# Performance work log

Measured on AMD Instinct MI355X. Metric: run time of the kernel, lower is better.

Reference implementation:

```python
import jax, jax.numpy as jnp
import numpy as np

DEPTH = 6
N_LEAVES = 2 ** DEPTH


def setup_inputs() -> dict:
    key = jax.random.key(0)
    ks = jax.random.split(key, 7)
    in_f, lw, out_f = 1024, 64, 512
    B = 4096
    s1 = 1.0 / np.sqrt(in_f)
    s2 = 1.0 / np.sqrt(lw)
    return {
        "x": jax.random.normal(ks[0], (B, in_f), jnp.float32),
        "node_weights": jax.random.uniform(ks[1], (N_LEAVES - 1, in_f), jnp.float32, -s1, s1),
        "node_biases": jax.random.uniform(ks[2], (N_LEAVES - 1, 1), jnp.float32, -s1, s1),
        "w1s": jax.random.uniform(ks[3], (N_LEAVES, in_f, lw), jnp.float32, -s1, s1),
        "b1s": jax.random.uniform(ks[4], (N_LEAVES, lw), jnp.float32, -s1, s1),
        "w2s": jax.random.uniform(ks[5], (N_LEAVES, lw, out_f), jnp.float32, -s2, s2),
        "b2s": jax.random.uniform(ks[6], (N_LEAVES, out_f), jnp.float32, -s2, s2),
    }


def _fff_forward(x, node_weights, node_biases, w1s, b1s, w2s, b2s):
    B = x.shape[0]
    # Soft routing: build per-leaf mixture weights level by level (training path).
    mixture = jnp.ones((B, N_LEAVES), x.dtype)
    for d in range(DEPTH):
        platform = 2 ** d - 1
        n_nodes = 2 ** d
        w = node_weights[platform:platform + n_nodes]          # (n, in)
        b = node_biases[platform:platform + n_nodes]            # (n, 1)
        logits = x @ w.T + b.T                                  # (B, n)
        be = jax.nn.sigmoid(logits)
        mod = jnp.stack([1.0 - be, be], axis=-1).reshape(B, 2 * n_nodes)
        mixture = (mixture.reshape(B, 2 * n_nodes, N_LEAVES // (2 * n_nodes))
                   * mod[:, :, None]).reshape(B, N_LEAVES)
    # All-leaf expert MLPs (grouped GEMMs), then mixture-weighted sum.
    h = jax.nn.relu(jnp.einsum('bi,liw->blw', x, w1s) + b1s[None])   # (B, L, W)
    y = jnp.einsum('blw,lwo->blo', h, w2s) + b2s[None]                # (B, L, O)
    return jnp.sum(y * mixture[:, :, None], axis=1)                   # (B, O)


def reference(x, node_weights, node_biases, w1s, b1s, w2s, b2s):
    return _fff_forward(x, node_weights, node_biases, w1s, b1s, w2s, b2s)
```

## Files before the change

kernel.cpp:

```cpp
#include <hip/hip_runtime.h>
#include <hip/hip_bf16.h>

typedef unsigned short u16;
typedef __attribute__((ext_vector_type(8))) short bf16x8;
typedef __attribute__((ext_vector_type(4))) float f32x4;
typedef __attribute__((ext_vector_type(16))) float f32x16;
typedef __attribute__((ext_vector_type(4))) unsigned short u16x4;
typedef __attribute__((ext_vector_type(8))) unsigned short u16x8;

#define BATCH 4096
#define INF   1024
#define NH    4096
#define OUTF  512
#define NLEAF 64
#define FDEPTH 6
#define ZSPL  4

__device__ __align__(16) u16  g_Xb[(size_t)BATCH * INF];
__device__ __align__(16) u16  g_W1t[(size_t)NH * INF];
__device__ __align__(16) u16  g_W2t[(size_t)OUTF * NH];
__device__ __align__(16) u16  g_NWh[(size_t)64 * INF];
__device__ __align__(16) u16  g_B2t[(size_t)OUTF * 64];
__device__ __align__(16) u16  g_Hb[(size_t)BATCH * NH];
__device__ __align__(16) float g_mix[(size_t)BATCH * NLEAF];
__device__ __align__(16) float g_part[(size_t)ZSPL * BATCH * OUTF];

__device__ inline u16 f2b(float f) {
  __hip_bfloat16 h = __float2bfloat16(f);
  return *reinterpret_cast<u16*>(&h);
}

__device__ inline void async16(const u16* g, u16* l) {
  __builtin_amdgcn_global_load_lds((const __attribute__((address_space(1))) void*)g,
                                   (__attribute__((address_space(3))) void*)l, 16, 0, 0);
}

__global__ __launch_bounds__(256) void prep_kernel(
    const float* __restrict__ x, const float* __restrict__ nw,
    const float* __restrict__ w1s, const float* __restrict__ w2s,
    const float* __restrict__ b2s) {
  __shared__ float tile[64 * 65];
  const int b = blockIdx.x;
  const int t = threadIdx.x;

  if (b < 2048) {
    int i = (b * 256 + t) * 8;
    float4 v0 = *(const float4*)(x + i);
    float4 v1 = *(const float4*)(x + i + 4);
    u16x8 h;
    h[0] = f2b(v0.x); h[1] = f2b(v0.y); h[2] = f2b(v0.z); h[3] = f2b(v0.w);
    h[4] = f2b(v1.x); h[5] = f2b(v1.y); h[6] = f2b(v1.z); h[7] = f2b(v1.w);
    *(u16x8*)(g_Xb + i) = h;
    return;
  }
  if (b < 2112) {
    int idx = ((b - 2048) * 256 + t) * 4;
    int n = idx >> 10;
    float4 v = make_float4(0.f, 0.f, 0.f, 0.f);
    if (n < 63) v = *(const float4*)(nw + idx);
    u16x4 h;
    h[0] = f2b(v.x); h[1] = f2b(v.y); h[2] = f2b(v.z); h[3] = f2b(v.w);
    *(u16x4*)(g_NWh + idx) = h;
    return;
  }

  const float* sb;
  u16* db;
  int R, C, r0, c0;
  if (b < 3136) {
    int idx = b - 2112;
    int z = idx >> 4;
    R = 1024; C = 64;
    r0 = (idx & 15) * 64; c0 = 0;
    sb = w1s + (size_t)z * R * C;
    db = g_W1t + (size_t)z * R * C;
  } else if (b < 3648) {
    int idx = b - 3136;
    R = 4096; C = 512;
    r0 = (idx >> 3) * 64; c0 = (idx & 7) * 64;
    sb = w2s;
    db = g_W2t;
  } else {
    int idx = b - 3648;
    R = 64; C = 512;
    r0 = 0; c0 = idx * 64;
    sb = b2s;
    db = g_B2t;
  }
  int cc4 = (t & 15) * 4;
#pragma unroll
  for (int it = 0; it < 4; ++it) {
    int rr = (t >> 4) + it * 16;
    float4 v = *(const float4*)(sb + (size_t)(r0 + rr) * C + c0 + cc4);
    tile[rr * 65 + cc4 + 0] = v.x;
    tile[rr * 65 + cc4 + 1] = v.y;
    tile[rr * 65 + cc4 + 2] = v.z;
    tile[rr * 65 + cc4 + 3] = v.w;
  }
  __syncthreads();
  int cc = t >> 2, rch = (t & 3) * 16;
  u16x8 o0, o1;
#pragma unroll
  for (int j = 0; j < 8; ++j) o0[j] = f2b(tile[(rch + j) * 65 + cc]);
#pragma unroll
  for (int j = 0; j < 8; ++j) o1[j] = f2b(tile[(rch + 8 + j) * 65 + cc]);
  u16* p = db + (size_t)(c0 + cc) * R + r0 + rch;
  *(u16x8*)p = o0;
  *(u16x8*)(p + 8) = o1;
}

__global__ __launch_bounds__(256) void mixture_kernel(
    const float* __restrict__ nb, float* __restrict__ out) {
  __shared__ __align__(16) unsigned char lds[57344];
  const int t = threadIdx.x;
  const int wv = t >> 6, ln = t & 63;
  const int quad = ln >> 4, m16 = ln & 15;
  const int r0 = blockIdx.x * 16;

  u16* stW = (u16*)(lds + wv * 10240);
  u16* stX = (u16*)(lds + wv * 10240 + 8192);
  float* lred = (float*)lds;
  float* ssig = (float*)(lds + 16384);
  u16* smixb = (u16*)(lds + 20480);
  u16* b2l = (u16*)(lds + 24576);

  f32x4 acc[4] = {};
#pragma unroll 1
  for (int it = 0; it < 4; ++it) {
    int kc = wv * 256 + it * 64;
#pragma unroll
    for (int j = 0; j < 8; ++j) {
      int id = j * 64 + ln;
      int row = id >> 3, c8 = (id & 7) ^ (row & 7);
      async16(g_NWh + (size_t)row * INF + kc + c8 * 8, stW + j * 512);
    }
#pragma unroll
    for (int j = 0; j < 2; ++j) {
      int id = j * 64 + ln;
      int row = id >> 3, c8 = (id & 7) ^ (row & 7);
      async16(g_Xb + (size_t)(r0 + row) * INF + kc + c8 * 8, stX + j * 512);
    }
    __syncthreads();
#pragma unroll
    for (int ks = 0; ks < 2; ++ks) {
      bf16x8 bF = *(const bf16x8*)(stX + m16 * 64 + ((ks * 4 + quad) ^ (m16 & 7)) * 8);
#pragma unroll
      for (int tw = 0; tw < 4; ++tw) {
        int row = tw * 16 + m16;
        bf16x8 aF = *(const bf16x8*)(stW + row * 64 + ((ks * 4 + quad) ^ (row & 7)) * 8);
        acc[tw] = __builtin_amdgcn_mfma_f32_16x16x32_bf16(aF, bF, acc[tw], 0, 0, 0);
      }
    }
    __syncthreads();
  }
#pragma unroll
  for (int tw = 0; tw < 4; ++tw)
#pragma unroll
    for (int r = 0; r < 4; ++r)
      lred[((size_t)wv * 64 + tw * 16 + quad * 4 + r) * 16 + m16] = acc[tw][r];
  __syncthreads();

#pragma unroll
  for (int j = 0; j < 8; ++j) {
    int id = (wv * 8 + j) * 64 + ln;
    int row = id >> 3, c8 = (id & 7) ^ (row & 7);
    async16(g_B2t + (size_t)row * 64 + c8 * 8, b2l + (wv * 8 + j) * 512);
  }

  {
    int n = t & 63, rg = t >> 6;
#pragma unroll
    for (int rr = 0; rr < 4; ++rr) {
      int row = rg * 4 + rr;
      float s = lred[(0 * 64 + n) * 16 + row] + lred[(1 * 64 + n) * 16 + row] +
                lred[(2 * 64 + n) * 16 + row] + lred[(3 * 64 + n) * 16 + row];
      if (n < 63) s += nb[n];
      ssig[row * 64 + n] = 1.f / (1.f + __expf(-s));
    }
  }
  __syncthreads();
  {
    int leaf = t & 63, rg = t >> 6;
#pragma unroll
    for (int rr = 0; rr < 4; ++rr) {
      int row = rg * 4 + rr;
      float p = 1.f;
#pragma unroll
      for (int d = 0; d < FDEPTH; ++d) {
        int node = (1 << d) - 1 + (leaf >> (FDEPTH - d));
        int bit = (leaf >> (FDEPTH - 1 - d)) & 1;
        float s = ssig[row * 64 + node];
        p *= bit ? s : (1.f - s);
      }
      g_mix[(size_t)(r0 + row) * 64 + leaf] = p;
      smixb[row * 64 + ((leaf >> 3) ^ (row & 7)) * 8 + (leaf & 7)] = f2b(p);
    }
  }
  __syncthreads();

  bf16x8 mixF[2];
#pragma unroll
  for (int ks = 0; ks < 2; ++ks)
    mixF[ks] = *(const bf16x8*)(smixb + m16 * 64 + ((ks * 4 + quad) ^ (m16 & 7)) * 8);
#pragma unroll 1
  for (int s = 0; s < 2; ++s) {
    f32x4 sacc[4] = {};
#pragma unroll
    for (int tile = 0; tile < 4; ++tile) {
#pragma unroll
      for (int ks = 0; ks < 2; ++ks) {
        int lrow = wv * 64 + tile * 16 + m16;
        bf16x8 aF = *(const bf16x8*)(b2l + lrow * 64 + ((ks * 4 + quad) ^ (lrow & 7)) * 8);
        sacc[tile] = __builtin_amdgcn_mfma_f32_16x16x32_bf16(aF, mixF[ks], sacc[tile], 0, 0, 0);
      }
    }
#pragma unroll
    for (int tile = 0; tile < 4; ++tile) {
      int o = s * 256 + wv * 64 + tile * 16 + quad * 4;
      *(f32x4*)(out + (size_t)(r0 + m16) * OUTF + o) = sacc[tile];
    }
    if (s == 0) {
      __syncthreads();
#pragma unroll
      for (int j = 0; j < 8; ++j) {
        int id = (wv * 8 + j) * 64 + ln;
        int row = id >> 3, c8 = (id & 7) ^ (row & 7);
        async16(g_B2t + (size_t)(256 + row) * 64 + c8 * 8, b2l + (wv * 8 + j) * 512);
      }
      __syncthreads();
    }
  }
}

__global__ __launch_bounds__(512, 2) void gemm1_kernel(const float* __restrict__ b1) {
  __shared__ __align__(16) u16 s_lds[65536];
  u16* lsA = s_lds;
  u16* lsB = s_lds + 32768;

  const int t = threadIdx.x;
  const int wv = t >> 6, ln = t & 63;
  const int quad = ln >> 4, m16 = ln & 15;
  const int wm = wv >> 2, wn = wv & 3;
  const int xcd = blockIdx.x & 7, slot = blockIdx.x >> 3;
  const int M0 = ((xcd >> 1) * 4 + (slot & 3)) * 256;
  const int N0 = ((xcd & 1) * 8 + (slot >> 2)) * 256;

  const int rhalf = ln >> 2;
  const int qg = (ln & 3) ^ ((ln >> 3) & 3);
  const u16* pA = g_W1t + (size_t)(M0 + wv * 32 + rhalf) * 1024 + qg * 8;
  const u16* pB = g_Xb + (size_t)(N0 + wv * 32 + rhalf) * 1024 + qg * 8;
  const int dst0 = wv * 1024;

  const int qx = (quad ^ ((m16 >> 1) & 3)) * 8;
  const int aro = (wm * 128 + m16) * 32 + qx;
  const int bro = (wn * 64 + m16) * 32 + qx;

  f32x4 acc[8][4] = {};
  bf16x8 bF[4];

#define STAGE_A(SLOT, TCOL)                                \
  do {                                                     \
    const u16* gs = pA + (TCOL);                           \
    u16* dd = lsA + (SLOT) * 8192 + dst0;                  \
    async16(gs, dd);                                       \
    async16(gs + 16 * 1024, dd + 512);                     \
  } while (0)
#define STAGE_B(SLOT, TCOL)                                \
  do {                                                     \
    const u16* gs = pB + (TCOL);                           \
    u16* dd = lsB + (SLOT) * 8192 + dst0;                  \
    async16(gs, dd);                                       \
    async16(gs + 16 * 1024, dd + 512);                     \
  } while (0)

#define G1_PHASE(ASLOT, BSLOT, AH, RELOAD_B, STAGE_STMT, VMCNT_STMT)        \
  {                                                                         \
    const u16* Abase = lsA + (ASLOT) * 8192;                                \
    bf16x8 aF[4];                                                           \
    _Pragma("unroll") for (int f = 0; f < 4; ++f)                           \
        aF[f] = *(const bf16x8*)(Abase + aro + ((AH) * 4 + f) * 512);       \
    if (RELOAD_B) {                                                         \
      const u16* Bbase = lsB + (BSLOT) * 8192;                              \
      _Pragma("unroll") for (int f = 0; f < 4; ++f)                         \
          bF[f] = *(const bf16x8*)(Bbase + bro + f * 512);                  \
    }                                                                       \
    STAGE_STMT;                                                             \
    __builtin_amdgcn_s_barrier();                                           \
    asm volatile("s_waitcnt lgkmcnt(0)" ::: "memory");                      \
    __builtin_amdgcn_s_setprio(1);                                          \
    _Pragma("unroll") for (int f = 0; f < 4; ++f)                           \
        _Pragma("unroll") for (int g = 0; g < 4; ++g)                       \
            acc[(AH) * 4 + f][g] = __builtin_amdgcn_mfma_f32_16x16x32_bf16( \
                aF[f], bF[g], acc[(AH) * 4 + f][g], 0, 0, 0);               \
    __builtin_amdgcn_s_setprio(0);                                          \
    VMCNT_STMT;                                                             \
    __builtin_amdgcn_s_barrier();                                           \
  }

  STAGE_B(0, 0);
  STAGE_A(0, 0);
  STAGE_B(1, 32);
  STAGE_A(1, 32);
  STAGE_B(2, 64);
  STAGE_A(2, 64);
  STAGE_B(3, 96);
  asm volatile("s_waitcnt vmcnt(6)" ::: "memory");
  __builtin_amdgcn_s_barrier();

#pragma unroll 1
  for (int i = 0; i < 8; ++i) {
    const int c1 = (2 * i + 1) * 64;
    const int c2 = ((2 * i + 2) & 15) * 64;
    const int c3 = ((2 * i + 3) & 15) * 64;
    G1_PHASE(0, 0, 0, 1, STAGE_A(3, c1 + 32), (void)0);
    G1_PHASE(0, 0, 1, 0, STAGE_B(0, c2), (void)0);
    G1_PHASE(1, 1, 0, 1, STAGE_A(0, c2), (void)0);
    G1_PHASE(1, 1, 1, 0, STAGE_B(1, c2 + 32),
             asm volatile("s_waitcnt vmcnt(6)" ::: "memory"));
    G1_PHASE(2, 2, 0, 1, STAGE_A(1, c2 + 32), (void)0);
    G1_PHASE(2, 2, 1, 0, STAGE_B(2, c3), (void)0);
    G1_PHASE(3, 3, 0, 1, STAGE_A(2, c3), (void)0);
    G1_PHASE(3, 3, 1, 0, STAGE_B(3, c3 + 32),
             asm volatile("s_waitcnt vmcnt(6)" ::: "memory"));
  }
#undef G1_PHASE
#undef STAGE_A
#undef STAGE_B

  asm volatile("s_waitcnt vmcnt(0)" ::: "memory");

  const int lb = (M0 >> 6) + wm * 2;
  float2 mx[4];
#pragma unroll
  for (int fb = 0; fb < 4; ++fb) {
    int bb = N0 + wn * 64 + fb * 16 + m16;
    mx[fb] = *(const float2*)(g_mix + (size_t)bb * 64 + lb);
  }
#pragma unroll
  for (int fa = 0; fa < 8; ++fa) {
    int n0 = M0 + wm * 128 + fa * 16 + quad * 4;
    float4 b1v = *(const float4*)(b1 + n0);
#pragma unroll
    for (int fb = 0; fb < 4; ++fb) {
      int bb = N0 + wn * 64 + fb * 16 + m16;
      float mixv = (fa < 4) ? mx[fb].x : mx[fb].y;
      u16x4 pk;
      pk[0] = f2b(fmaxf(acc[fa][fb][0] + b1v.x, 0.f) * mixv);
      pk[1] = f2b(fmaxf(acc[fa][fb][1] + b1v.y, 0.f) * mixv);
      pk[2] = f2b(fmaxf(acc[fa][fb][2] + b1v.z, 0.f) * mixv);
      pk[3] = f2b(fmaxf(acc[fa][fb][3] + b1v.w, 0.f) * mixv);
      *(u16x4*)(g_Hb + (size_t)bb * NH + n0) = pk;
    }
  }
}

__global__ __launch_bounds__(256) void gemm2_kernel() {
  constexpr int BM = 128, BN = 128, BK = 64, K = 4096, LD = 4096;

  __shared__ u16 lsA[BM * BK];
  __shared__ u16 lsB[BN * BK];

  const int bid = blockIdx.x;
  const int xcd = bid & 7, slot = bid >> 3;
  const int zidx = xcd >> 1;
  const int ytile = (xcd & 1) * 16 + (slot & 15);
  const int xtile = slot >> 4;

  const int t = threadIdx.x;
  const int wv = t >> 6, ln = t & 63;
  const int wm = wv >> 1, wn = wv & 1;
  const int quad = ln >> 4, m16 = ln & 15;
  const int am0 = ytile * BM;
  const int bn0 = xtile * BN;
  const int kbeg = zidx * (K / ZSPL);
  const int kend = kbeg + K / ZSPL;

  f32x4 acc[4][4] = {};

  for (int kc = kbeg; kc < kend; kc += BK) {
#pragma unroll
    for (int i = 0; i < 4; ++i) {
      int id = i * 256 + t;
      int row = id >> 3;
      int c8 = (id & 7) ^ (row & 7);
      async16(g_Hb + (size_t)(am0 + row) * LD + kc + c8 * 8, lsA + (i * 256 + wv * 64) * 8);
    }
#pragma unroll
    for (int i = 0; i < 4; ++i) {
      int id = i * 256 + t;
      int row = id >> 3;
      int c8 = (id & 7) ^ (row & 7);
      async16(g_W2t + (size_t)(bn0 + row) * LD + kc + c8 * 8, lsB + (i * 256 + wv * 64) * 8);
    }
    __syncthreads();
#pragma unroll
    for (int ks = 0; ks < 2; ++ks) {
      bf16x8 wF[4], xF[4];
#pragma unroll
      for (int tw = 0; tw < 4; ++tw) {
        int row = wn * 64 + tw * 16 + m16;
        wF[tw] = *(const bf16x8*)(lsB + row * BK + ((ks * 4 + quad) ^ (row & 7)) * 8);
      }
#pragma unroll
      for (int tb = 0; tb < 4; ++tb) {
        int row = wm * 64 + tb * 16 + m16;
        xF[tb] = *(const bf16x8*)(lsA + row * BK + ((ks * 4 + quad) ^ (row & 7)) * 8);
      }
#pragma unroll
      for (int tw = 0; tw < 4; ++tw)
#pragma unroll
        for (int tb = 0; tb < 4; ++tb)
          acc[tw][tb] = __builtin_amdgcn_mfma_f32_16x16x32_bf16(wF[tw], xF[tb], acc[tw][tb], 0, 0, 0);
    }
    __syncthreads();
  }

  float* part = g_part + (size_t)zidx * ((size_t)BATCH * OUTF);
#pragma unroll
  for (int tw = 0; tw < 4; ++tw) {
    int og = bn0 + wn * 64 + tw * 16 + quad * 4;
#pragma unroll
    for (int tb = 0; tb < 4; ++tb) {
      int bg = am0 + wm * 64 + tb * 16 + m16;
      *(f32x4*)(part + (size_t)bg * OUTF + og) = acc[tw][tb];
    }
  }
}

__global__ __launch_bounds__(256) void reduce_kernel(float* __restrict__ out) {
  int i = (blockIdx.x * 256 + threadIdx.x) * 4;
  float4 s = *(const float4*)(out + i);
#pragma unroll
  for (int z = 0; z < ZSPL; ++z) {
    const float4 p = *(const float4*)(g_part + (size_t)z * BATCH * OUTF + i);
    s.x += p.x; s.y += p.y; s.z += p.z; s.w += p.w;
  }
  *(float4*)(out + i) = s;
}

extern "C" void kernel_launch(void* const* d_in, const int* in_sizes, int n_in,
                              void* d_out, int out_size, void* d_ws, size_t ws_size,
                              hipStream_t stream) {
  const float* x = (const float*)d_in[0];
  const float* nw = (const float*)d_in[1];
  const float* nb = (const float*)d_in[2];
  const float* w1s = (const float*)d_in[3];
  const float* b1s = (const float*)d_in[4];
  const float* w2s = (const float*)d_in[5];
  const float* b2s = (const float*)d_in[6];
  float* out = (float*)d_out;
  (void)d_ws; (void)ws_size;

  hipLaunchKernelGGL(prep_kernel, dim3(3656), dim3(256), 0, stream,
                     x, nw, w1s, w2s, b2s);
  hipLaunchKernelGGL(mixture_kernel, dim3(256), dim3(256), 0, stream, nb, out);
  hipLaunchKernelGGL(gemm1_kernel, dim3(256), dim3(512), 0, stream, b1s);
  hipLaunchKernelGGL(gemm2_kernel, dim3(512), dim3(256), 0, stream);
  hipLaunchKernelGGL(reduce_kernel, dim3(2048), dim3(256), 0, stream, out);
}
```

Measured before the change: 191.9 us.

## Rewrite gemm2 as a 4-stage async-pipelined 256x128 tile kernel with 512 threads

Replaces the single-buffered 128x128 gemm2 (sync before and after each K chunk) with a 256x128 output tile per 512-thread block. The K loop now runs through a 4-slot LDS ring of async global-to-LDS copies, uses explicit vmcnt/lgkmcnt waits and raised priority around the MFMA bursts, and issues each prefetch while the previous slot is being computed. The aim is to hide global load latency and raise arithmetic intensity per block. In exchange it uses 96KB of LDS per block and halves the grid to 256 blocks, which can limit occupancy. It also relies on a delicate hand-written wait-count schedule.

```diff
diff --git a/kernel.cpp b/kernel.cpp
--- a/kernel.cpp
+++ b/kernel.cpp
@@ -354,75 +354,115 @@
   }
 }
 
-__global__ __launch_bounds__(256) void gemm2_kernel() {
-  constexpr int BM = 128, BN = 128, BK = 64, K = 4096, LD = 4096;
-
-  __shared__ u16 lsA[BM * BK];
-  __shared__ u16 lsB[BN * BK];
-
-  const int bid = blockIdx.x;
-  const int xcd = bid & 7, slot = bid >> 3;
-  const int zidx = xcd >> 1;
-  const int ytile = (xcd & 1) * 16 + (slot & 15);
-  const int xtile = slot >> 4;
+__global__ __launch_bounds__(512, 2) void gemm2_kernel() {
+  __shared__ __align__(16) u16 s_lds[49152];
+  u16* lsA = s_lds;
+  u16* lsB = s_lds + 32768;
 
   const int t = threadIdx.x;
   const int wv = t >> 6, ln = t & 63;
-  const int wm = wv >> 1, wn = wv & 1;
   const int quad = ln >> 4, m16 = ln & 15;
-  const int am0 = ytile * BM;
-  const int bn0 = xtile * BN;
-  const int kbeg = zidx * (K / ZSPL);
-  const int kend = kbeg + K / ZSPL;
-
-  f32x4 acc[4][4] = {};
-
-  for (int kc = kbeg; kc < kend; kc += BK) {
-#pragma unroll
-    for (int i = 0; i < 4; ++i) {
-      int id = i * 256 + t;
-      int row = id >> 3;
-      int c8 = (id & 7) ^ (row & 7);
-      async16(g_Hb + (size_t)(am0 + row) * LD + kc + c8 * 8, lsA + (i * 256 + wv * 64) * 8);
-    }
-#pragma unroll
-    for (int i = 0; i < 4; ++i) {
-      int id = i * 256 + t;
-      int row = id >> 3;
-      int c8 = (id & 7) ^ (row & 7);
-      async16(g_W2t + (size_t)(bn0 + row) * LD + kc + c8 * 8, lsB + (i * 256 + wv * 64) * 8);
-    }
-    __syncthreads();
-#pragma unroll
-    for (int ks = 0; ks < 2; ++ks) {
-      bf16x8 wF[4], xF[4];
-#pragma unroll
-      for (int tw = 0; tw < 4; ++tw) {
-        int row = wn * 64 + tw * 16 + m16;
-        wF[tw] = *(const bf16x8*)(lsB + row * BK + ((ks * 4 + quad) ^ (row & 7)) * 8);
-      }
-#pragma unroll
-      for (int tb = 0; tb < 4; ++tb) {
-        int row = wm * 64 + tb * 16 + m16;
-        xF[tb] = *(const bf16x8*)(lsA + row * BK + ((ks * 4 + quad) ^ (row & 7)) * 8);
-      }
-#pragma unroll
-      for (int tw = 0; tw < 4; ++tw)
-#pragma unroll
-        for (int tb = 0; tb < 4; ++tb)
-          acc[tw][tb] = __builtin_amdgcn_mfma_f32_16x16x32_bf16(wF[tw], xF[tb], acc[tw][tb], 0, 0, 0);
-    }
-    __syncthreads();
-  }
+  const int wm = wv >> 2, wn = wv & 3;
+  const int xcd = blockIdx.x & 7, slot = blockIdx.x >> 3;
+  const int btile = xcd * 4 + (slot >> 3);
+  const int rem = slot & 7;
+  const int mtile = rem & 1, zidx = rem >> 1;
+  const int N0 = btile * 128;
+  const int M0 = mtile * 256;
+  const int kbeg = zidx * 1024;
+
+  const int rhalf = ln >> 2;
+  const int qg = (ln & 3) ^ ((ln >> 3) & 3);
+  const u16* pA = g_W2t + (size_t)(M0 + wv * 32 + rhalf) * 4096 + kbeg + qg * 8;
+  const u16* pB = g_Hb + (size_t)(N0 + wv * 16 + rhalf) * 4096 + kbeg + qg * 8;
+  const int dstA = wv * 1024;
+  const int dstB = wv * 512;
+
+  const int qx = (quad ^ ((m16 >> 1) & 3)) * 8;
+  const int aro = (wm * 128 + m16) * 32 + qx;
+  const int bro = (wn * 32 + m16) * 32 + qx;
+
+  f32x4 acc[8][2] = {};
+  bf16x8 bF[2];
+
+#define STAGE_A2(SLOT, TCOL)                               \
+  do {                                                     \
+    const u16* gs = pA + (TCOL);                           \
+    u16* dd = lsA + (SLOT) * 8192 + dstA;                  \
+    async16(gs, dd);                                       \
+    async16(gs + 16 * 4096, dd + 512);                     \
+  } while (0)
+#define STAGE_B2(SLOT, TCOL)                               \
+  do {                                                     \
+    const u16* gs = pB + (TCOL);                           \
+    u16* dd = lsB + (SLOT) * 4096 + dstB;                  \
+    async16(gs, dd);                                       \
+  } while (0)
+
+#define G2_PHASE(ASLOT, BSLOT, AH, RELOAD_B, STAGE_STMT, VMCNT_STMT)        \
+  {                                                                         \
+    const u16* Abase = lsA + (ASLOT) * 8192;                                \
+    bf16x8 aF[4];                                                           \
+    _Pragma("unroll") for (int f = 0; f < 4; ++f)                           \
+        aF[f] = *(const bf16x8*)(Abase + aro + ((AH) * 4 + f) * 512);       \
+    if (RELOAD_B) {                                                         \
+      const u16* Bbase = lsB + (BSLOT) * 4096;                              \
+      _Pragma("unroll") for (int g = 0; g < 2; ++g)                         \
+          bF[g] = *(const bf16x8*)(Bbase + bro + g * 512);                  \
+    }                                                                       \
+    STAGE_STMT;                                                             \
+    __builtin_amdgcn_s_barrier();                                           \
+    asm volatile("s_waitcnt lgkmcnt(0)" ::: "memory");                      \
+    __builtin_amdgcn_s_setprio(1);                                          \
+    _Pragma("unroll") for (int f = 0; f < 4; ++f)                           \
+        _Pragma("unroll") for (int g = 0; g < 2; ++g)                       \
+            acc[(AH) * 4 + f][g] = __builtin_amdgcn_mfma_f32_16x16x32_bf16( \
+                aF[f], bF[g], acc[(AH) * 4 + f][g], 0, 0, 0);               \
+    __builtin_amdgcn_s_setprio(0);                                          \
+    VMCNT_STMT;                                                             \
+    __builtin_amdgcn_s_barrier();                                           \
+  }
+
+  STAGE_B2(0, 0);
+  STAGE_A2(0, 0);
+  STAGE_B2(1, 32);
+  STAGE_A2(1, 32);
+  STAGE_B2(2, 64);
+  STAGE_A2(2, 64);
+  STAGE_B2(3, 96);
+  asm volatile("s_waitcnt vmcnt(4)" ::: "memory");
+  __builtin_amdgcn_s_barrier();
+
+#pragma unroll 1
+  for (int i = 0; i < 8; ++i) {
+    const int c1 = (2 * i + 1) * 64;
+    const int c2 = ((2 * i + 2) & 15) * 64;
+    const int c3 = ((2 * i + 3) & 15) * 64;
+    G2_PHASE(0, 0, 0, 1, STAGE_A2(3, c1 + 32), (void)0);
+    G2_PHASE(0, 0, 1, 0, STAGE_B2(0, c2), (void)0);
+    G2_PHASE(1, 1, 0, 1, STAGE_A2(0, c2), (void)0);
+    G2_PHASE(1, 1, 1, 0, STAGE_B2(1, c2 + 32),
+             asm volatile("s_waitcnt vmcnt(4)" ::: "memory"));
+    G2_PHASE(2, 2, 0, 1, STAGE_A2(1, c2 + 32), (void)0);
+    G2_PHASE(2, 2, 1, 0, STAGE_B2(2, c3), (void)0);
+    G2_PHASE(3, 3, 0, 1, STAGE_A2(2, c3), (void)0);
+    G2_PHASE(3, 3, 1, 0, STAGE_B2(3, c3 + 32),
+             asm volatile("s_waitcnt vmcnt(4)" ::: "memory"));
+  }
+#undef G2_PHASE
+#undef STAGE_A2
+#undef STAGE_B2
+
+  asm volatile("s_waitcnt vmcnt(0)" ::: "memory");
 
   float* part = g_part + (size_t)zidx * ((size_t)BATCH * OUTF);
 #pragma unroll
-  for (int tw = 0; tw < 4; ++tw) {
-    int og = bn0 + wn * 64 + tw * 16 + quad * 4;
-#pragma unroll
-    for (int tb = 0; tb < 4; ++tb) {
-      int bg = am0 + wm * 64 + tb * 16 + m16;
-      *(f32x4*)(part + (size_t)bg * OUTF + og) = acc[tw][tb];
+  for (int fa = 0; fa < 8; ++fa) {
+    int og = M0 + wm * 128 + fa * 16 + quad * 4;
+#pragma unroll
+    for (int fb = 0; fb < 2; ++fb) {
+      int bg = N0 + wn * 32 + fb * 16 + m16;
+      *(f32x4*)(part + (size_t)bg * OUTF + og) = acc[fa][fb];
     }
   }
 }
@@ -455,6 +495,6 @@
                      x, nw, w1s, w2s, b2s);
   hipLaunchKernelGGL(mixture_kernel, dim3(256), dim3(256), 0, stream, nb, out);
   hipLaunchKernelGGL(gemm1_kernel, dim3(256), dim3(512), 0, stream, b1s);
-  hipLaunchKernelGGL(gemm2_kernel, dim3(512), dim3(256), 0, stream);
+  hipLaunchKernelGGL(gemm2_kernel, dim3(256), dim3(512), 0, stream);
   hipLaunchKernelGGL(reduce_kernel, dim3(2048), dim3(256), 0, stream, out);
 }
```

New measurement: 188.5 us (median of 3 runs). About the same (-1.8%).
